# Optimization experiments

Measured on AMD Instinct MI355X. Metric: run time of the kernel, lower is better.

The kernel has to match this reference:

```python
import jax, jax.numpy as jnp
import numpy as np

E1 = 150000   # number of 1-hop edges
E2 = 150000   # number of 2-hop edges
T = 400000    # triangles per triangle class
C = 64        # in_channels
H = 64        # mlp_hidden_channels
L = 2         # num DR2FWL2Conv layers
N_MLP = 8     # MLPs per conv layer


def setup_inputs() -> dict:
    key = jax.random.key(0)
    ks = jax.random.split(key, 20)
    edge_attr = jax.random.normal(ks[0], (E1, C), jnp.float32)
    edge_attr2 = jax.random.normal(ks[1], (E2, C), jnp.float32)
    # triangle index tensors: rows (ij, ik, kj); hop type of each row decides the range
    triangle_1_1_1 = jax.random.randint(ks[2], (3, T), 0, E1)
    triangle_1_1_2 = jnp.stack([jax.random.randint(jax.random.fold_in(ks[3], r), (T,), 0, m)
                                for r, m in enumerate([E1, E1, E2])])
    triangle_1_2_2 = jnp.stack([jax.random.randint(jax.random.fold_in(ks[4], r), (T,), 0, m)
                                for r, m in enumerate([E1, E2, E2])])
    triangle_2_2_2 = jax.random.randint(ks[5], (3, T), 0, E2)
    inverse_edge_1 = jax.random.permutation(ks[6], E1)
    inverse_edge_2 = jax.random.permutation(ks[7], E2)
    s = 0.05
    mlp_w1 = jax.random.normal(ks[8], (L, N_MLP, C, H), jnp.float32) * s
    mlp_b1 = jnp.zeros((L, N_MLP, H), jnp.float32)
    mlp_w2 = jax.random.normal(ks[9], (L, N_MLP, H, C), jnp.float32) * s
    mlp_b2 = jnp.zeros((L, N_MLP, C), jnp.float32)
    lin_w1 = jax.random.normal(ks[10], (C, C), jnp.float32) * s
    lin_b1 = jnp.zeros((C,), jnp.float32)
    lin_w2 = jax.random.normal(ks[11], (C, C), jnp.float32) * s
    lin_b2 = jnp.zeros((C,), jnp.float32)
    return dict(edge_attr=edge_attr, edge_attr2=edge_attr2,
                triangle_1_1_1=triangle_1_1_1, triangle_1_1_2=triangle_1_1_2,
                triangle_1_2_2=triangle_1_2_2, triangle_2_2_2=triangle_2_2_2,
                inverse_edge_1=inverse_edge_1, inverse_edge_2=inverse_edge_2,
                mlp_w1=mlp_w1, mlp_b1=mlp_b1, mlp_w2=mlp_w2, mlp_b2=mlp_b2,
                lin_w1=lin_w1, lin_b1=lin_b1, lin_w2=lin_w2, lin_b2=lin_b2)


def reference(edge_attr, edge_attr2, triangle_1_1_1, triangle_1_1_2,
              triangle_1_2_2, triangle_2_2_2, inverse_edge_1, inverse_edge_2,
              mlp_w1, mlp_b1, mlp_w2, mlp_b2, lin_w1, lin_b1, lin_w2, lin_b2):
    eps = 0.0
    eps2 = 0.0
    ij111, ik111, kj111 = triangle_1_1_1
    ij112, ik112, kj112 = triangle_1_1_2
    ij122, ik122, kj122 = triangle_1_2_2
    ij222, ik222, kj222 = triangle_2_2_2
    seg = jax.ops.segment_sum

    e1, e2 = edge_attr, edge_attr2
    n1, n2 = e1.shape[0], e2.shape[0]
    for li in range(mlp_w1.shape[0]):
        def mlp(x, mi, li=li):
            h = jax.nn.relu(x @ mlp_w1[li, mi] + mlp_b1[li, mi])
            return h @ mlp_w2[li, mi] + mlp_b2[li, mi]
        m111 = seg(mlp(e1[ik111], 0) * mlp(e1[kj111], 0), ij111, num_segments=n1)
        m112 = seg(mlp(e1[ik112], 1) * mlp(e2[kj112], 2), ij112, num_segments=n1)
        m122 = seg(mlp(e2[ik122], 3) * mlp(e2[kj122], 3), ij122, num_segments=n1)
        e1 = e1 * (1.0 + eps) + m111 + m112 + m112[inverse_edge_1] + m122
        m211 = seg(mlp(e1[ij112], 4) * mlp(e1[ik112], 4), kj112, num_segments=n2)
        m212 = seg(mlp(e1[ij122], 5) * mlp(e2[kj122], 6), ik122, num_segments=n2)
        m222 = seg(mlp(e2[ik222], 7) * mlp(e2[kj222], 7), ij222, num_segments=n2)
        e2 = e2 * (1.0 + eps2) + m211 + m212 + m212[inverse_edge_2] + m222
        # norm=None (Identity), relu after, dropout=0 in eval
        e1, e2 = jax.nn.relu(e1), jax.nn.relu(e2)
    return (e1 @ lin_w1 + lin_b1, e2 @ lin_w2 + lin_b2)
```

## Files before the change

### kernel.cpp

```cpp
#include <hip/hip_runtime.h>
#include <hip/hip_fp16.h>


typedef unsigned short u16;
typedef unsigned int u32;
typedef _Float16 f16;
typedef __attribute__((ext_vector_type(8))) short s16x8;
typedef __attribute__((ext_vector_type(4))) float f32x4;
typedef __attribute__((ext_vector_type(4))) _Float16 f16x4;

#define MFMA16(a, b, c) __builtin_amdgcn_mfma_f32_16x16x32_bf16((a), (b), (c), 0, 0, 0)

static __device__ __forceinline__ u16 bf16_rne(float x) {
  u32 u = __float_as_uint(x);
  return (u16)((u + 0x7fffu + ((u >> 16) & 1u)) >> 16);
}
static __device__ __forceinline__ float bf16_f32(u16 h) {
  return __uint_as_float(((u32)h) << 16);
}
static __device__ __forceinline__ void cvt_hilo8(const f32x4 a, const f32x4 b, s16x8& hi, s16x8& lo) {
#pragma unroll
  for (int j = 0; j < 4; j++) {
    float x = a[j];
    u16 h = bf16_rne(x);
    u16 l = bf16_rne(x - bf16_f32(h));
    hi[j] = (short)h; lo[j] = (short)l;
  }
#pragma unroll
  for (int j = 0; j < 4; j++) {
    float x = b[j];
    u16 h = bf16_rne(x);
    u16 l = bf16_rne(x - bf16_f32(h));
    hi[4 + j] = (short)h; lo[4 + j] = (short)l;
  }
}

__global__ __launch_bounds__(256) void repack_split_kernel(const float* __restrict__ src,
                                                           u16* __restrict__ hi, u16* __restrict__ lo, int nmat) {
  int o = blockIdx.x * 256 + threadIdx.x;
  int stride = gridDim.x * 256;
  int total = nmat * 4096;
  for (; o < total; o += stride) {
    int m = o >> 12, r = o & 4095;
    int j = r & 7, lane = (r >> 3) & 63, nt = (r >> 9) & 3, kt = (r >> 11) & 1;
    int k = kt * 32 + ((lane >> 4) << 3) + j;
    int n = nt * 16 + (lane & 15);
    float x = src[(size_t)m * 4096 + k * 64 + n];
    u16 h = bf16_rne(x);
    hi[o] = h;
    lo[o] = bf16_rne(x - bf16_f32(h));
  }
}

__global__ __launch_bounds__(256) void copy_kernel(const float* __restrict__ src, float* __restrict__ dst, int n4) {
  int i = blockIdx.x * 256 + threadIdx.x;
  int stride = gridDim.x * 256;
  const f32x4* s4 = (const f32x4*)src;
  f32x4* d4 = (f32x4*)dst;
  for (; i < n4; i += stride) d4[i] = s4[i];
}

__global__ __launch_bounds__(256) void relu_kernel(float* __restrict__ e, int n4) {
  int i = blockIdx.x * 256 + threadIdx.x;
  int stride = gridDim.x * 256;
  f32x4* e4 = (f32x4*)e;
  for (; i < n4; i += stride) {
    f32x4 v = e4[i];
#pragma unroll
    for (int j = 0; j < 4; j++) v[j] = fmaxf(v[j], 0.0f);
    e4[i] = v;
  }
}

template <bool DO_RELU>
__global__ __launch_bounds__(256) void addinv2_kernel(float* __restrict__ e, const f16* __restrict__ A,
                                                      const f16* __restrict__ B, const int* __restrict__ inv, int E) {
  int i = blockIdx.x * 256 + threadIdx.x;
  int stride = gridDim.x * 256;
  int total = E * 16;
  f32x4* e4 = (f32x4*)e;
  const f16x4* A4 = (const f16x4*)A;
  const f16x4* B4 = (const f16x4*)B;
  for (; i < total; i += stride) {
    int r = i >> 4, q = i & 15;
    int ir = inv[r];
    f32x4 v = e4[i];
    f16x4 a = A4[i];
    f16x4 b = B4[i];
    f16x4 bi = B4[(size_t)ir * 16 + q];
#pragma unroll
    for (int j = 0; j < 4; j++) {
      float x = v[j] + (float)a[j] + (float)b[j] + (float)bi[j];
      v[j] = DO_RELU ? fmaxf(x, 0.0f) : x;
    }
    e4[i] = v;
  }
}

__global__ __launch_bounds__(256) void seg3_kernel(
    __half2* __restrict__ dstA, __half2* __restrict__ dstB,
    const __half2* __restrict__ paA, const __half2* __restrict__ pbA,
    const int* __restrict__ iA0, const int* __restrict__ iA1, const int* __restrict__ iA2,
    const __half2* __restrict__ paB, const __half2* __restrict__ pbB,
    const int* __restrict__ iB0, const int* __restrict__ iB1, const int* __restrict__ iB2,
    const __half2* __restrict__ paC, const __half2* __restrict__ pbC,
    const int* __restrict__ iC0, const int* __restrict__ iC1, const int* __restrict__ iC2,
    int T) {
  int i = blockIdx.x * 256 + threadIdx.x;
  int stride = gridDim.x * 256;
  int total = 3 * T * 32;
  for (; i < total; i += stride) {
    int u = i >> 5, cp = i & 31;
    __half2* dst;
    const __half2 *pa, *pb;
    const int *i0, *i1, *i2;
    int t;
    if (u < T) { t = u; dst = dstA; pa = paA; pb = pbA; i0 = iA0; i1 = iA1; i2 = iA2; }
    else if (u < 2 * T) { t = u - T; dst = dstB; pa = paB; pb = pbB; i0 = iB0; i1 = iB1; i2 = iB2; }
    else { t = u - 2 * T; dst = dstA; pa = paC; pb = pbC; i0 = iC0; i1 = iC1; i2 = iC2; }
    __half2 va = pa[(size_t)i1[t] * 32 + cp];
    __half2 vb = pb[(size_t)i2[t] * 32 + cp];
    float2 fa = __half22float2(va), fb = __half22float2(vb);
    __half2 prod = __floats2half2_rn(fa.x * fb.x, fa.y * fb.y);
    unsafeAtomicAdd(&dst[(size_t)i0[t] * 32 + cp], prod);
  }
}

__global__ __launch_bounds__(256) void mlpN_kernel(
    const float* __restrict__ e1s, const float* __restrict__ e2s,
    f16* __restrict__ d0, f16* __restrict__ d1, f16* __restrict__ d2,
    f16* __restrict__ d3, f16* __restrict__ d4, f16* __restrict__ d5,
    const u16* __restrict__ w1h_, const u16* __restrict__ w1l_,
    const u16* __restrict__ w2h_, const u16* __restrict__ w2l_,
    const float* __restrict__ b1_, const float* __restrict__ b2_,
    int miPacked, int selMask, int nUnits, int s1, int s2, int BPU) {
  __shared__ float hshm[4][1024];
  const int u = blockIdx.x / BPU;
  if (u >= nUnits) return;
  const int tid = threadIdx.x;
  const int wave = tid >> 6, lane = tid & 63;
  const int lrow = lane & 15, lk = lane >> 4;

  const int mi = (miPacked >> (4 * u)) & 15;
  const int sel = (selMask >> u) & 1;
  const float* src = sel ? e2s : e1s;
  const int strips = sel ? s2 : s1;
  f16* dst = (u == 0) ? d0 : (u == 1) ? d1 : (u == 2) ? d2 : (u == 3) ? d3 : (u == 4) ? d4 : d5;

  const s16x8* W1H = (const s16x8*)(w1h_ + (size_t)mi * 4096);
  const s16x8* W1L = (const s16x8*)(w1l_ + (size_t)mi * 4096);
  const s16x8* W2H = (const s16x8*)(w2h_ + (size_t)mi * 4096);
  const s16x8* W2L = (const s16x8*)(w2l_ + (size_t)mi * 4096);
  s16x8 w1h[2][4], w1l[2][4], w2h[2][4], w2l[2][4];
#pragma unroll
  for (int kt = 0; kt < 2; kt++)
#pragma unroll
    for (int nt = 0; nt < 4; nt++) {
      const int f = (kt * 4 + nt) * 64 + lane;
      w1h[kt][nt] = W1H[f];
      w1l[kt][nt] = W1L[f];
      w2h[kt][nt] = W2H[f];
      w2l[kt][nt] = W2L[f];
    }
  float bias1[4], bias2[4];
#pragma unroll
  for (int nt = 0; nt < 4; nt++) {
    bias1[nt] = b1_[mi * 64 + nt * 16 + lrow];
    bias2[nt] = b2_[mi * 64 + nt * 16 + lrow];
  }

  float* hl = hshm[wave];
  const int lb = blockIdx.x % BPU;
  for (int strip = lb * 4 + wave; strip < strips; strip += BPU * 4) {
    const float* xp = src + (size_t)(strip * 16 + lrow) * 64 + lk * 8;
    f32x4 x0 = *(const f32x4*)(xp + 0);
    f32x4 x1 = *(const f32x4*)(xp + 4);
    f32x4 x2 = *(const f32x4*)(xp + 32);
    f32x4 x3 = *(const f32x4*)(xp + 36);
    s16x8 ah[2], al[2];
    cvt_hilo8(x0, x1, ah[0], al[0]);
    cvt_hilo8(x2, x3, ah[1], al[1]);

    f32x4 acc[4];
#pragma unroll
    for (int nt = 0; nt < 4; nt++) { acc[nt][0] = bias1[nt]; acc[nt][1] = bias1[nt]; acc[nt][2] = bias1[nt]; acc[nt][3] = bias1[nt]; }
#pragma unroll
    for (int kt = 0; kt < 2; kt++)
#pragma unroll
      for (int nt = 0; nt < 4; nt++) {
        acc[nt] = MFMA16(ah[kt], w1h[kt][nt], acc[nt]);
        acc[nt] = MFMA16(ah[kt], w1l[kt][nt], acc[nt]);
        acc[nt] = MFMA16(al[kt], w1h[kt][nt], acc[nt]);
      }

#pragma unroll
    for (int nt = 0; nt < 4; nt++)
#pragma unroll
      for (int r = 0; r < 4; r++) {
        const int row = lk * 4 + r;
        const int col = nt * 16 + lrow;
        hl[row * 64 + (col ^ ((row & 7) << 2))] = fmaxf(acc[nt][r], 0.0f);
      }
    s16x8 bh[2], bl[2];
#pragma unroll
    for (int kt = 0; kt < 2; kt++) {
      const int colb = kt * 32 + lk * 8;
      const int xr = (lrow & 7) << 2;
      f32x4 h0 = *(const f32x4*)&hl[lrow * 64 + ((colb + 0) ^ xr)];
      f32x4 h1 = *(const f32x4*)&hl[lrow * 64 + ((colb + 4) ^ xr)];
      cvt_hilo8(h0, h1, bh[kt], bl[kt]);
    }

    f32x4 out[4];
#pragma unroll
    for (int nt = 0; nt < 4; nt++) { out[nt][0] = bias2[nt]; out[nt][1] = bias2[nt]; out[nt][2] = bias2[nt]; out[nt][3] = bias2[nt]; }
#pragma unroll
    for (int kt = 0; kt < 2; kt++)
#pragma unroll
      for (int nt = 0; nt < 4; nt++) {
        out[nt] = MFMA16(bh[kt], w2h[kt][nt], out[nt]);
        out[nt] = MFMA16(bh[kt], w2l[kt][nt], out[nt]);
        out[nt] = MFMA16(bl[kt], w2h[kt][nt], out[nt]);
      }

    f16* dp = dst + (size_t)strip * 1024;
#pragma unroll
    for (int nt = 0; nt < 4; nt++)
#pragma unroll
      for (int r = 0; r < 4; r++)
        dp[(lk * 4 + r) * 64 + nt * 16 + lrow] = (f16)out[nt][r];
  }
}

template <bool RELU>
__global__ __launch_bounds__(256) void lin_kernel(const float* __restrict__ src, float* __restrict__ dst,
                                                  const u16* __restrict__ wh_, const u16* __restrict__ wl_,
                                                  const float* __restrict__ b_, int nstrips) {
  const int tid = threadIdx.x;
  const int wave = tid >> 6, lane = tid & 63;
  const int lrow = lane & 15, lk = lane >> 4;

  const s16x8* WH = (const s16x8*)wh_;
  const s16x8* WL = (const s16x8*)wl_;
  s16x8 wh[2][4], wl[2][4];
#pragma unroll
  for (int kt = 0; kt < 2; kt++)
#pragma unroll
    for (int nt = 0; nt < 4; nt++) {
      const int f = (kt * 4 + nt) * 64 + lane;
      wh[kt][nt] = WH[f];
      wl[kt][nt] = WL[f];
    }
  float bias[4];
#pragma unroll
  for (int nt = 0; nt < 4; nt++) bias[nt] = b_[nt * 16 + lrow];

  for (int s = blockIdx.x * 4 + wave; s < nstrips; s += gridDim.x * 4) {
    const float* xp = src + (size_t)(s * 16 + lrow) * 64 + lk * 8;
    f32x4 x0 = *(const f32x4*)(xp + 0);
    f32x4 x1 = *(const f32x4*)(xp + 4);
    f32x4 x2 = *(const f32x4*)(xp + 32);
    f32x4 x3 = *(const f32x4*)(xp + 36);
    if (RELU) {
#pragma unroll
      for (int j = 0; j < 4; j++) {
        x0[j] = fmaxf(x0[j], 0.0f); x1[j] = fmaxf(x1[j], 0.0f);
        x2[j] = fmaxf(x2[j], 0.0f); x3[j] = fmaxf(x3[j], 0.0f);
      }
    }
    s16x8 ah[2], al[2];
    cvt_hilo8(x0, x1, ah[0], al[0]);
    cvt_hilo8(x2, x3, ah[1], al[1]);

    f32x4 acc[4];
#pragma unroll
    for (int nt = 0; nt < 4; nt++) { acc[nt][0] = bias[nt]; acc[nt][1] = bias[nt]; acc[nt][2] = bias[nt]; acc[nt][3] = bias[nt]; }
#pragma unroll
    for (int kt = 0; kt < 2; kt++)
#pragma unroll
      for (int nt = 0; nt < 4; nt++) {
        acc[nt] = MFMA16(ah[kt], wh[kt][nt], acc[nt]);
        acc[nt] = MFMA16(ah[kt], wl[kt][nt], acc[nt]);
        acc[nt] = MFMA16(al[kt], wh[kt][nt], acc[nt]);
      }
    float* dp = dst + (size_t)s * 1024;
#pragma unroll
    for (int nt = 0; nt < 4; nt++)
#pragma unroll
      for (int r = 0; r < 4; r++)
        dp[(lk * 4 + r) * 64 + nt * 16 + lrow] = acc[nt][r];
  }
}

extern "C" void kernel_launch(void* const* d_in, const int* in_sizes, int n_in,
                              void* d_out, int out_size, void* d_ws, size_t ws_size,
                              hipStream_t stream) {
  const float* in_e1 = (const float*)d_in[0];
  const float* in_e2 = (const float*)d_in[1];
  const int* t111 = (const int*)d_in[2];
  const int* t112 = (const int*)d_in[3];
  const int* t122 = (const int*)d_in[4];
  const int* t222 = (const int*)d_in[5];
  const int* inv1 = (const int*)d_in[6];
  const int* inv2 = (const int*)d_in[7];
  const float* mw1 = (const float*)d_in[8];
  const float* mb1 = (const float*)d_in[9];
  const float* mw2 = (const float*)d_in[10];
  const float* mb2 = (const float*)d_in[11];
  const float* lw1 = (const float*)d_in[12];
  const float* lb1 = (const float*)d_in[13];
  const float* lw2 = (const float*)d_in[14];
  const float* lb2 = (const float*)d_in[15];

  const int E1 = in_sizes[0] / 64, E2 = in_sizes[1] / 64;
  const int T = in_sizes[2] / 3;
  const int L = in_sizes[8] / (8 * 64 * 64);
  const size_t nE1 = (size_t)E1 * 64, nE2 = (size_t)E2 * 64;
  const size_t nMax = nE1 > nE2 ? nE1 : nE2;

  float* e1b = (float*)d_ws;
  float* e2b = e1b + nE1;
  f16* mA = (f16*)(e2b + nE2);
  f16* mB = mA + nMax;
  f16* q0 = mB + nMax;
  f16* q1 = q0 + nE1;
  const size_t wmat = (size_t)L * 8 * 4096;
  u16* w1h = (u16*)(q1 + nE1);
  u16* w1l = w1h + wmat;
  u16* w2h = w1l + wmat;
  u16* w2l = w2h + wmat;
  u16* lwh = w2l + wmat;
  u16* lwl = lwh + 8192;
  const size_t needB = (nE1 + nE2) * 4 + (2 * nMax + 2 * nE1) * 2 + (4 * wmat + 4 * 4096) * 2 + 64;
  if (ws_size < needB) return;

  f16* q2 = (f16*)d_out;
  f16* q3 = q2 + nE2;
  f16* q6 = q3 + nE2;
  f16* q7 = q6 + nE2;
  f16* q4 = q0;
  f16* q5 = q1;

  const int s1 = E1 / 16, s2 = E2 / 16;
  const int SEGB = 2048, ELTB = 2048, BPU = 256, LINB = 256;

  repack_split_kernel<<<256, 256, 0, stream>>>(mw1, w1h, w1l, L * 8);
  repack_split_kernel<<<256, 256, 0, stream>>>(mw2, w2h, w2l, L * 8);
  repack_split_kernel<<<32, 256, 0, stream>>>(lw1, lwh, lwl, 1);
  repack_split_kernel<<<32, 256, 0, stream>>>(lw2, lwh + 4096, lwl + 4096, 1);
  copy_kernel<<<ELTB, 256, 0, stream>>>(in_e1, e1b, (int)(nE1 / 4));
  copy_kernel<<<ELTB, 256, 0, stream>>>(in_e2, e2b, (int)(nE2 / 4));

  for (int li = 0; li < L; li++) {
    const u16* W1H = w1h + (size_t)li * 8 * 4096;
    const u16* W1L = w1l + (size_t)li * 8 * 4096;
    const u16* W2H = w2h + (size_t)li * 8 * 4096;
    const u16* W2L = w2l + (size_t)li * 8 * 4096;
    const float* B1 = mb1 + (size_t)li * 8 * 64;
    const float* B2 = mb2 + (size_t)li * 8 * 64;

    mlpN_kernel<<<6 * BPU, 256, 0, stream>>>(e1b, e2b, q0, q1, q2, q3, q6, q7,
                                             W1H, W1L, W2H, W2L, B1, B2,
                                             0x763210, 0x3C, 6, s1, s2, BPU);
    hipMemsetAsync(mA, 0, 2 * nMax * 2, stream);
    seg3_kernel<<<SEGB, 256, 0, stream>>>(
        (__half2*)mA, (__half2*)mB,
        (const __half2*)q0, (const __half2*)q0, t111, t111 + T, t111 + 2 * T,
        (const __half2*)q1, (const __half2*)q2, t112, t112 + T, t112 + 2 * T,
        (const __half2*)q3, (const __half2*)q3, t122, t122 + T, t122 + 2 * T, T);
    addinv2_kernel<false><<<ELTB, 256, 0, stream>>>(e1b, mA, mB, inv1, E1);

    mlpN_kernel<<<2 * BPU, 256, 0, stream>>>(e1b, e2b, q4, q5, q2, q3, q6, q7,
                                             W1H, W1L, W2H, W2L, B1, B2,
                                             0x54, 0x0, 2, s1, s2, BPU);
    if (li < L - 1) relu_kernel<<<ELTB, 256, 0, stream>>>(e1b, (int)(nE1 / 4));

    hipMemsetAsync(mA, 0, 2 * nMax * 2, stream);
    seg3_kernel<<<SEGB, 256, 0, stream>>>(
        (__half2*)mA, (__half2*)mB,
        (const __half2*)q4, (const __half2*)q4, t112 + 2 * T, t112, t112 + T,
        (const __half2*)q5, (const __half2*)q6, t122 + T, t122, t122 + 2 * T,
        (const __half2*)q7, (const __half2*)q7, t222, t222 + T, t222 + 2 * T, T);
    addinv2_kernel<true><<<ELTB, 256, 0, stream>>>(e2b, mA, mB, inv2, E2);
  }

  lin_kernel<true><<<LINB, 256, 0, stream>>>(e1b, (float*)d_out, lwh, lwl, lb1, s1);
  lin_kernel<false><<<LINB, 256, 0, stream>>>(e2b, (float*)d_out + nE1, lwh + 4096, lwl + 4096, lb2, s2);
}
```

Baseline: 896.1 us.

## Store edge features in fp16 and accumulate segment sums directly into them

The persistent edge feature buffers e1/e2 switch from fp32 to fp16, which halves their traffic in the MLP, elementwise and linear kernels. The seg3 atomics for two of the three triangle classes now add straight into the edge buffer, so one scratch buffer, part of the memset and one read in the add-inverse kernel go away. The cost is lower precision for the residual state and for accumulation, since fp16 atomics now add into the running features and that error carries across layers.

After: 818.6 us. 8.6% less time.

```diff
diff --git a/kernel.cpp b/kernel.cpp
--- a/kernel.cpp
+++ b/kernel.cpp
@@ -7,7 +7,7 @@
 typedef _Float16 f16;
 typedef __attribute__((ext_vector_type(8))) short s16x8;
 typedef __attribute__((ext_vector_type(4))) float f32x4;
-typedef __attribute__((ext_vector_type(4))) _Float16 f16x4;
+typedef __attribute__((ext_vector_type(8))) _Float16 f16x8;
 
 #define MFMA16(a, b, c) __builtin_amdgcn_mfma_f32_16x16x32_bf16((a), (b), (c), 0, 0, 0)
 
@@ -18,20 +18,13 @@
 static __device__ __forceinline__ float bf16_f32(u16 h) {
   return __uint_as_float(((u32)h) << 16);
 }
-static __device__ __forceinline__ void cvt_hilo8(const f32x4 a, const f32x4 b, s16x8& hi, s16x8& lo) {
-#pragma unroll
-  for (int j = 0; j < 4; j++) {
-    float x = a[j];
+static __device__ __forceinline__ void cvt_hilo8_f16(const f16x8 v, s16x8& hi, s16x8& lo) {
+#pragma unroll
+  for (int j = 0; j < 8; j++) {
+    float x = (float)v[j];
     u16 h = bf16_rne(x);
-    u16 l = bf16_rne(x - bf16_f32(h));
-    hi[j] = (short)h; lo[j] = (short)l;
-  }
-#pragma unroll
-  for (int j = 0; j < 4; j++) {
-    float x = b[j];
-    u16 h = bf16_rne(x);
-    u16 l = bf16_rne(x - bf16_f32(h));
-    hi[4 + j] = (short)h; lo[4 + j] = (short)l;
+    hi[j] = (short)h;
+    lo[j] = (short)bf16_rne(x - bf16_f32(h));
   }
 }
 
@@ -52,48 +45,52 @@
   }
 }
 
-__global__ __launch_bounds__(256) void copy_kernel(const float* __restrict__ src, float* __restrict__ dst, int n4) {
+__global__ __launch_bounds__(256) void cvtcopy_kernel(const float* __restrict__ src, f16* __restrict__ dst, int n8) {
   int i = blockIdx.x * 256 + threadIdx.x;
   int stride = gridDim.x * 256;
   const f32x4* s4 = (const f32x4*)src;
-  f32x4* d4 = (f32x4*)dst;
-  for (; i < n4; i += stride) d4[i] = s4[i];
-}
-
-__global__ __launch_bounds__(256) void relu_kernel(float* __restrict__ e, int n4) {
+  f16x8* d8 = (f16x8*)dst;
+  for (; i < n8; i += stride) {
+    f32x4 a = s4[2 * i], b = s4[2 * i + 1];
+    f16x8 o;
+#pragma unroll
+    for (int j = 0; j < 4; j++) { o[j] = (f16)a[j]; o[4 + j] = (f16)b[j]; }
+    d8[i] = o;
+  }
+}
+
+__global__ __launch_bounds__(256) void relu16_kernel(f16* __restrict__ e, int n8) {
   int i = blockIdx.x * 256 + threadIdx.x;
   int stride = gridDim.x * 256;
-  f32x4* e4 = (f32x4*)e;
-  for (; i < n4; i += stride) {
-    f32x4 v = e4[i];
-#pragma unroll
-    for (int j = 0; j < 4; j++) v[j] = fmaxf(v[j], 0.0f);
-    e4[i] = v;
+  f16x8* e8 = (f16x8*)e;
+  for (; i < n8; i += stride) {
+    f16x8 v = e8[i];
+#pragma unroll
+    for (int j = 0; j < 8; j++) v[j] = v[j] > (f16)0 ? v[j] : (f16)0;
+    e8[i] = v;
   }
 }
 
 template <bool DO_RELU>
-__global__ __launch_bounds__(256) void addinv2_kernel(float* __restrict__ e, const f16* __restrict__ A,
-                                                      const f16* __restrict__ B, const int* __restrict__ inv, int E) {
+__global__ __launch_bounds__(256) void addinvB_kernel(f16* __restrict__ e, const f16* __restrict__ B,
+                                                      const int* __restrict__ inv, int E) {
   int i = blockIdx.x * 256 + threadIdx.x;
   int stride = gridDim.x * 256;
-  int total = E * 16;
-  f32x4* e4 = (f32x4*)e;
-  const f16x4* A4 = (const f16x4*)A;
-  const f16x4* B4 = (const f16x4*)B;
+  int total = E * 8;
+  f16x8* e8 = (f16x8*)e;
+  const f16x8* B8 = (const f16x8*)B;
   for (; i < total; i += stride) {
-    int r = i >> 4, q = i & 15;
+    int r = i >> 3, q = i & 7;
     int ir = inv[r];
-    f32x4 v = e4[i];
-    f16x4 a = A4[i];
-    f16x4 b = B4[i];
-    f16x4 bi = B4[(size_t)ir * 16 + q];
-#pragma unroll
-    for (int j = 0; j < 4; j++) {
-      float x = v[j] + (float)a[j] + (float)b[j] + (float)bi[j];
-      v[j] = DO_RELU ? fmaxf(x, 0.0f) : x;
-    }
-    e4[i] = v;
+    f16x8 ev = e8[i];
+    f16x8 bv = B8[i];
+    f16x8 biv = B8[(size_t)ir * 8 + q];
+#pragma unroll
+    for (int j = 0; j < 8; j++) {
+      float x = (float)ev[j] + (float)bv[j] + (float)biv[j];
+      ev[j] = (f16)(DO_RELU ? fmaxf(x, 0.0f) : x);
+    }
+    e8[i] = ev;
   }
 }
 
@@ -127,7 +124,7 @@
 }
 
 __global__ __launch_bounds__(256) void mlpN_kernel(
-    const float* __restrict__ e1s, const float* __restrict__ e2s,
+    const f16* __restrict__ e1s, const f16* __restrict__ e2s,
     f16* __restrict__ d0, f16* __restrict__ d1, f16* __restrict__ d2,
     f16* __restrict__ d3, f16* __restrict__ d4, f16* __restrict__ d5,
     const u16* __restrict__ w1h_, const u16* __restrict__ w1l_,
@@ -143,7 +140,7 @@
 
   const int mi = (miPacked >> (4 * u)) & 15;
   const int sel = (selMask >> u) & 1;
-  const float* src = sel ? e2s : e1s;
+  const f16* src = sel ? e2s : e1s;
   const int strips = sel ? s2 : s1;
   f16* dst = (u == 0) ? d0 : (u == 1) ? d1 : (u == 2) ? d2 : (u == 3) ? d3 : (u == 4) ? d4 : d5;
 
@@ -172,14 +169,12 @@
   float* hl = hshm[wave];
   const int lb = blockIdx.x % BPU;
   for (int strip = lb * 4 + wave; strip < strips; strip += BPU * 4) {
-    const float* xp = src + (size_t)(strip * 16 + lrow) * 64 + lk * 8;
-    f32x4 x0 = *(const f32x4*)(xp + 0);
-    f32x4 x1 = *(const f32x4*)(xp + 4);
-    f32x4 x2 = *(const f32x4*)(xp + 32);
-    f32x4 x3 = *(const f32x4*)(xp + 36);
+    const f16* xp = src + (size_t)(strip * 16 + lrow) * 64 + lk * 8;
+    f16x8 xa = *(const f16x8*)(xp);
+    f16x8 xb = *(const f16x8*)(xp + 32);
     s16x8 ah[2], al[2];
-    cvt_hilo8(x0, x1, ah[0], al[0]);
-    cvt_hilo8(x2, x3, ah[1], al[1]);
+    cvt_hilo8_f16(xa, ah[0], al[0]);
+    cvt_hilo8_f16(xb, ah[1], al[1]);
 
     f32x4 acc[4];
 #pragma unroll
@@ -208,7 +203,20 @@
       const int xr = (lrow & 7) << 2;
       f32x4 h0 = *(const f32x4*)&hl[lrow * 64 + ((colb + 0) ^ xr)];
       f32x4 h1 = *(const f32x4*)&hl[lrow * 64 + ((colb + 4) ^ xr)];
-      cvt_hilo8(h0, h1, bh[kt], bl[kt]);
+      s16x8 hi, lo;
+#pragma unroll
+      for (int j = 0; j < 4; j++) {
+        float x = h0[j];
+        u16 h = bf16_rne(x);
+        hi[j] = (short)h; lo[j] = (short)bf16_rne(x - bf16_f32(h));
+      }
+#pragma unroll
+      for (int j = 0; j < 4; j++) {
+        float x = h1[j];
+        u16 h = bf16_rne(x);
+        hi[4 + j] = (short)h; lo[4 + j] = (short)bf16_rne(x - bf16_f32(h));
+      }
+      bh[kt] = hi; bl[kt] = lo;
     }
 
     f32x4 out[4];
@@ -233,7 +241,7 @@
 }
 
 template <bool RELU>
-__global__ __launch_bounds__(256) void lin_kernel(const float* __restrict__ src, float* __restrict__ dst,
+__global__ __launch_bounds__(256) void lin_kernel(const f16* __restrict__ src, float* __restrict__ dst,
                                                   const u16* __restrict__ wh_, const u16* __restrict__ wl_,
                                                   const float* __restrict__ b_, int nstrips) {
   const int tid = threadIdx.x;
@@ -256,21 +264,19 @@
   for (int nt = 0; nt < 4; nt++) bias[nt] = b_[nt * 16 + lrow];
 
   for (int s = blockIdx.x * 4 + wave; s < nstrips; s += gridDim.x * 4) {
-    const float* xp = src + (size_t)(s * 16 + lrow) * 64 + lk * 8;
-    f32x4 x0 = *(const f32x4*)(xp + 0);
-    f32x4 x1 = *(const f32x4*)(xp + 4);
-    f32x4 x2 = *(const f32x4*)(xp + 32);
-    f32x4 x3 = *(const f32x4*)(xp + 36);
+    const f16* xp = src + (size_t)(s * 16 + lrow) * 64 + lk * 8;
+    f16x8 xa = *(const f16x8*)(xp);
+    f16x8 xb = *(const f16x8*)(xp + 32);
     if (RELU) {
 #pragma unroll
-      for (int j = 0; j < 4; j++) {
-        x0[j] = fmaxf(x0[j], 0.0f); x1[j] = fmaxf(x1[j], 0.0f);
-        x2[j] = fmaxf(x2[j], 0.0f); x3[j] = fmaxf(x3[j], 0.0f);
+      for (int j = 0; j < 8; j++) {
+        xa[j] = xa[j] > (f16)0 ? xa[j] : (f16)0;
+        xb[j] = xb[j] > (f16)0 ? xb[j] : (f16)0;
       }
     }
     s16x8 ah[2], al[2];
-    cvt_hilo8(x0, x1, ah[0], al[0]);
-    cvt_hilo8(x2, x3, ah[1], al[1]);
+    cvt_hilo8_f16(xa, ah[0], al[0]);
+    cvt_hilo8_f16(xb, ah[1], al[1]);
 
     f32x4 acc[4];
 #pragma unroll
@@ -318,10 +324,9 @@
   const size_t nE1 = (size_t)E1 * 64, nE2 = (size_t)E2 * 64;
   const size_t nMax = nE1 > nE2 ? nE1 : nE2;
 
-  float* e1b = (float*)d_ws;
-  float* e2b = e1b + nE1;
-  f16* mA = (f16*)(e2b + nE2);
-  f16* mB = mA + nMax;
+  f16* e1b = (f16*)d_ws;
+  f16* e2b = e1b + nE1;
+  f16* mB = e2b + nE2;
   f16* q0 = mB + nMax;
   f16* q1 = q0 + nE1;
   const size_t wmat = (size_t)L * 8 * 4096;
@@ -331,7 +336,7 @@
   u16* w2l = w2h + wmat;
   u16* lwh = w2l + wmat;
   u16* lwl = lwh + 8192;
-  const size_t needB = (nE1 + nE2) * 4 + (2 * nMax + 2 * nE1) * 2 + (4 * wmat + 4 * 4096) * 2 + 64;
+  const size_t needB = (nE1 + nE2 + nMax + 2 * nE1) * 2 + (4 * wmat + 4 * 4096) * 2 + 64;
   if (ws_size < needB) return;
 
   f16* q2 = (f16*)d_out;
@@ -348,8 +353,8 @@
   repack_split_kernel<<<256, 256, 0, stream>>>(mw2, w2h, w2l, L * 8);
   repack_split_kernel<<<32, 256, 0, stream>>>(lw1, lwh, lwl, 1);
   repack_split_kernel<<<32, 256, 0, stream>>>(lw2, lwh + 4096, lwl + 4096, 1);
-  copy_kernel<<<ELTB, 256, 0, stream>>>(in_e1, e1b, (int)(nE1 / 4));
-  copy_kernel<<<ELTB, 256, 0, stream>>>(in_e2, e2b, (int)(nE2 / 4));
+  cvtcopy_kernel<<<ELTB, 256, 0, stream>>>(in_e1, e1b, (int)(nE1 / 8));
+  cvtcopy_kernel<<<ELTB, 256, 0, stream>>>(in_e2, e2b, (int)(nE2 / 8));
 
   for (int li = 0; li < L; li++) {
     const u16* W1H = w1h + (size_t)li * 8 * 4096;
@@ -362,26 +367,26 @@
     mlpN_kernel<<<6 * BPU, 256, 0, stream>>>(e1b, e2b, q0, q1, q2, q3, q6, q7,
                                              W1H, W1L, W2H, W2L, B1, B2,
                                              0x763210, 0x3C, 6, s1, s2, BPU);
-    hipMemsetAsync(mA, 0, 2 * nMax * 2, stream);
+    hipMemsetAsync(mB, 0, nE1 * 2, stream);
     seg3_kernel<<<SEGB, 256, 0, stream>>>(
-        (__half2*)mA, (__half2*)mB,
+        (__half2*)e1b, (__half2*)mB,
         (const __half2*)q0, (const __half2*)q0, t111, t111 + T, t111 + 2 * T,
         (const __half2*)q1, (const __half2*)q2, t112, t112 + T, t112 + 2 * T,
         (const __half2*)q3, (const __half2*)q3, t122, t122 + T, t122 + 2 * T, T);
-    addinv2_kernel<false><<<ELTB, 256, 0, stream>>>(e1b, mA, mB, inv1, E1);
+    addinvB_kernel<false><<<ELTB, 256, 0, stream>>>(e1b, mB, inv1, E1);
 
     mlpN_kernel<<<2 * BPU, 256, 0, stream>>>(e1b, e2b, q4, q5, q2, q3, q6, q7,
                                              W1H, W1L, W2H, W2L, B1, B2,
                                              0x54, 0x0, 2, s1, s2, BPU);
-    if (li < L - 1) relu_kernel<<<ELTB, 256, 0, stream>>>(e1b, (int)(nE1 / 4));
-
-    hipMemsetAsync(mA, 0, 2 * nMax * 2, stream);
+    if (li < L - 1) relu16_kernel<<<ELTB, 256, 0, stream>>>(e1b, (int)(nE1 / 8));
+
+    hipMemsetAsync(mB, 0, nE2 * 2, stream);
     seg3_kernel<<<SEGB, 256, 0, stream>>>(
-        (__half2*)mA, (__half2*)mB,
+        (__half2*)e2b, (__half2*)mB,
         (const __half2*)q4, (const __half2*)q4, t112 + 2 * T, t112, t112 + T,
         (const __half2*)q5, (const __half2*)q6, t122 + T, t122, t122 + 2 * T,
         (const __half2*)q7, (const __half2*)q7, t222, t222 + T, t222 + 2 * T, T);
-    addinv2_kernel<true><<<ELTB, 256, 0, stream>>>(e2b, mA, mB, inv2, E2);
+    addinvB_kernel<true><<<ELTB, 256, 0, stream>>>(e2b, mB, inv2, E2);
   }
 
   lin_kernel<true><<<LINB, 256, 0, stream>>>(e1b, (float*)d_out, lwh, lwl, lb1, s1);
```
